# Optimization experiments

Measured on AMD Instinct MI355X. Metric: run time of the kernel, lower is better.

## Reference

```python
import jax, jax.numpy as jnp
import numpy as np

N = 100000   # nodes
E = 800000   # edges (avg degree 8)
IN = 128     # in_dim
H = 128      # hidden_dim
L = 3        # num_layers
EPS = 1e-5   # torch LayerNorm default


def setup_inputs() -> dict:
    key = jax.random.key(0)
    ks = jax.random.split(key, 10)
    s = 0.05
    # DAG edge list: src < dst guarantees acyclicity and node N-1 is a sink.
    rng = np.random.default_rng(0)
    src = rng.integers(0, N - 1, size=E)
    dst = src + 1 + (rng.random(E) * (N - 1 - src)).astype(np.int64)
    return {
        "node_feats": jax.random.normal(ks[0], (N, IN), jnp.float32),
        "src": jnp.asarray(src, jnp.int32),
        "dst": jnp.asarray(dst, jnp.int32),
        "W_in": jax.random.normal(ks[1], (IN, H), jnp.float32) * s,
        "b_in": jnp.zeros((H,), jnp.float32),
        "Ws": jax.random.normal(ks[2], (L, H, H), jnp.float32) * s,
        "bs": jnp.zeros((L, H), jnp.float32),
        "Wn": jax.random.normal(ks[3], (L, H, H), jnp.float32) * s,
        "bn": jnp.zeros((L, H), jnp.float32),
        "Wg": jax.random.normal(ks[4], (L, 2 * H, H), jnp.float32) * s,
        "bg": jnp.zeros((L, H), jnp.float32),
        "gamma": jnp.ones((L, H), jnp.float32),
        "beta": jnp.zeros((L, H), jnp.float32),
        "W_att": jax.random.normal(ks[5], (H, H), jnp.float32) * s,
        "b_att": jnp.zeros((H,), jnp.float32),
        "W_score": jax.random.normal(ks[6], (H, 1), jnp.float32) * s,
        "b_score": jnp.zeros((1,), jnp.float32),
    }


def reference(node_feats, src, dst, W_in, b_in, Ws, bs, Wn, bn, Wg, bg,
              gamma, beta, W_att, b_att, W_score, b_score):
    n = node_feats.shape[0]
    ones_e = jnp.ones(src.shape, node_feats.dtype)
    indeg = jax.ops.segment_sum(ones_e, dst, num_segments=n)          # [N]
    has_pred = (indeg > 0).astype(node_feats.dtype)[:, None]          # [N,1]
    inv_deg = (1.0 / jnp.maximum(indeg, 1.0))[:, None]                # [N,1]
    outdeg = jax.ops.segment_sum(ones_e, src, num_segments=n)
    sink_mask = outdeg == 0                                           # [N]

    h = node_feats @ W_in + b_in                                      # [N,H]
    for i in range(Ws.shape[0]):
        hs = h @ Ws[i] + bs[i]
        # predecessor mean of layer-input h (no within-layer recurrence)
        neigh = jax.ops.segment_sum(h[src], dst, num_segments=n) * inv_deg
        hn = neigh @ Wn[i] + bn[i]
        m = hs + has_pred * hn  # nodes with no preds use m = hs only (bias too)
        gate = jax.nn.sigmoid(jnp.concatenate([h, m], axis=-1) @ Wg[i] + bg[i])
        v = gate * m + (1.0 - gate) * h
        mu = v.mean(-1, keepdims=True)
        var = ((v - mu) ** 2).mean(-1, keepdims=True)
        v = (v - mu) * jax.lax.rsqrt(var + EPS) * gamma[i] + beta[i]
        h = jax.nn.relu(v)

    # attention pooling over sink nodes only
    a = jnp.tanh(h @ W_att + b_att)
    scores = (a @ W_score)[:, 0] + b_score[0]
    scores = jnp.where(sink_mask, scores, -jnp.inf)
    w = jax.nn.softmax(scores, axis=0)  # zero weight on non-sinks
    graph_emb = (w[:, None] * h).sum(0)
    return h, graph_emb
```

## Files before the change

### kernel.cpp

```cpp
#include <hip/hip_runtime.h>
#include <cmath>

typedef unsigned short u16;
typedef unsigned int   u32;
typedef __attribute__((ext_vector_type(8))) short bf16x8;
typedef __attribute__((ext_vector_type(4))) float f32x4;
typedef __attribute__((ext_vector_type(4))) u32   u32x4;

__device__ __forceinline__ float bf2f(u16 u){
    union { u32 i; float f; } x; x.i = ((u32)u) << 16; return x.f;
}
__device__ __forceinline__ u16 f2bf(float f){
    union { float f; u32 i; } x; x.f = f;
    u32 r = x.i + 0x7fffu + ((x.i >> 16) & 1u);
    return (u16)(r >> 16);
}

__device__ __forceinline__ size_t frag_idx(int n, int k){
    int t = n >> 4, sl = n & 15, kk = k >> 5, g16 = (k >> 3) & 3, e = k & 7;
    return ((size_t)(t*4 + kk)*64 + g16*16 + sl)*8 + e;
}


__global__ void k_count(const int* __restrict__ src, const int* __restrict__ dst,
                        int* cnt, int* notsink, int* pos, int E){
    int e = blockIdx.x*256 + threadIdx.x;
    if (e < E){
        pos[e] = atomicAdd(&cnt[dst[e]], 1);
        notsink[src[e]] = 1;
    }
}

__global__ void k_sinklist(const int* __restrict__ notsink, int* sink_list,
                           int* nsink, int N){
    int i = blockIdx.x*256 + threadIdx.x;
    if (i < N && notsink[i] == 0){
        int p = atomicAdd(nsink, 1);
        sink_list[p] = i;
    }
}

__global__ void k_scan1(const int* __restrict__ in, int* blocksum, int N){
    __shared__ int sh[256];
    int tid = threadIdx.x;
    int base = blockIdx.x*1024 + tid*4;
    int s = 0;
    for (int j=0;j<4;j++){ int i = base+j; s += (i < N) ? in[i] : 0; }
    sh[tid] = s; __syncthreads();
    for (int d=128; d>0; d>>=1){ if (tid < d) sh[tid] += sh[tid+d]; __syncthreads(); }
    if (tid == 0) blocksum[blockIdx.x] = sh[0];
}

__global__ void k_scan2(int* blocksum, int nb){
    if (threadIdx.x == 0){
        int run = 0;
        for (int i=0;i<nb;i++){ int v = blocksum[i]; blocksum[i] = run; run += v; }
    }
}

__global__ void k_scan3(const int* __restrict__ in, const int* __restrict__ blockoff,
                        int* out, float* inv_deg, float* haspred, int N){
    __shared__ int sh[256];
    int tid = threadIdx.x;
    int base = blockIdx.x*1024 + tid*4;
    int e[4]; int s = 0;
    for (int j=0;j<4;j++){ int i = base+j; e[j] = (i < N) ? in[i] : 0; s += e[j]; }
    sh[tid] = s; __syncthreads();
    for (int d=1; d<256; d<<=1){
        int t = (tid >= d) ? sh[tid-d] : 0;
        __syncthreads();
        sh[tid] += t;
        __syncthreads();
    }
    int excl = sh[tid] - s + blockoff[blockIdx.x];
    for (int j=0;j<4;j++){
        int i = base+j;
        if (i < N){
            out[i] = excl; excl += e[j];
            inv_deg[i] = 1.0f / (float)(e[j] > 1 ? e[j] : 1);
            haspred[i] = e[j] > 0 ? 1.0f : 0.0f;
        }
    }
}

__global__ void k_place(const int* __restrict__ src, const int* __restrict__ dst,
                        const int* __restrict__ row_ptr, const int* __restrict__ pos,
                        int* csr_src, int E){
    int e = blockIdx.x*256 + threadIdx.x;
    if (e < E)
        csr_src[row_ptr[dst[e]] + pos[e]] = src[e];
}

__global__ void k_wt_plain(const float* __restrict__ W_in, const float* __restrict__ W_att,
                           const float* __restrict__ Ws, const float* __restrict__ Wn,
                           u16* WT_in, u16* WT_att, u16* WB){
    int i = blockIdx.x*256 + threadIdx.x;
    if (i < 32768){
        const float* srcm = (i < 16384) ? W_in : W_att;
        u16* dstm = (i < 16384) ? WT_in : WT_att;
        int w = i & 16383, n = w >> 7, k = w & 127;
        dstm[n*128 + k] = f2bf(srcm[k*128 + n]);
    } else {
        int off = i - 32768;
        int m  = off / 49152;
        int w  = off % 49152;
        int l  = w >> 14, ww = w & 16383;
        int n  = ww >> 7, k = ww & 127;
        const float* srcm = m ? Wn : Ws;
        u16* dstm = WB + ((size_t)l*2 + m)*32768;
        dstm[frag_idx(n, k)] = f2bf(srcm[(size_t)l*16384 + k*128 + n]);
    }
}

__global__ void k_wt_comp(const float* __restrict__ Ws, const float* __restrict__ Wn,
                          const float* __restrict__ Wg,
                          const float* __restrict__ bs, const float* __restrict__ bn,
                          u16* WB, float* vb){
    __shared__ float cols[2][128];
    int l = blockIdx.x / 129;
    int b = blockIdx.x % 129;
    const float* Wgb = Wg + (size_t)l*32768 + 16384;
    int tid = threadIdx.x;
    if (b == 128){
        int n = tid & 127;
        const float* bv = (tid < 128) ? (bs + l*128) : (bn + l*128);
        float acc = 0.f;
        for (int j=0;j<128;j++) acc += bv[j] * Wgb[j*128 + n];
        vb[l*256 + (tid>>7)*128 + n] = acc;
        return;
    }
    int m  = b >> 6;
    int n0 = (b & 63) * 2;
    int nn = tid >> 7, k = tid & 127;
    cols[tid>>7][tid&127] = Wgb[(size_t)(tid&127)*128 + n0 + (tid>>7)];
    __syncthreads();
    const float* A = (m ? Wn : Ws) + (size_t)l*16384;
    float acc = 0.f;
    for (int j=0;j<128;j++) acc += A[k*128 + j] * cols[nn][j];
    int n = n0 + nn;
    if (m == 0) acc += Wg[(size_t)l*32768 + k*128 + n];
    u16* dstm = WB + ((size_t)l*2 + m)*32768;
    dstm[frag_idx(128 + n, k)] = f2bf(acc);
}


__global__ void k_neigh(const u16* __restrict__ h, const int* __restrict__ row_ptr,
                        const int* __restrict__ indeg, const float* __restrict__ inv_deg,
                        const int* __restrict__ csr_src, u16* __restrict__ neigh, int N){
    int wid  = (blockIdx.x*256 + threadIdx.x) >> 6;
    int lane = threadIdx.x & 63;
    int sub = lane >> 4, sl = lane & 15;
    int node = wid*4 + sub;
    bool valid = node < N;
    int deg   = valid ? indeg[node]   : 0;
    int start = valid ? row_ptr[node] : 0;
    float acc[8] = {0.f,0.f,0.f,0.f,0.f,0.f,0.f,0.f};
    for (int e0 = 0; __any(e0 < deg); e0 += 16){
        int idx = 0;
        if (e0 + sl < deg) idx = csr_src[start + e0 + sl];
        int cnt = deg - e0;
        #pragma unroll
        for (int j = 0; j < 16; j++){
            int sidx = __shfl(idx, (sub << 4) | j);
            if (j < cnt){
                bf16x8 v = *(const bf16x8*)(h + (size_t)sidx*128 + sl*8);
                #pragma unroll
                for (int t=0;t<8;t++) acc[t] += bf2f((u16)v[t]);
            }
        }
    }
    if (valid){
        float iv = inv_deg[node];
        u16 o[8];
        #pragma unroll
        for (int t=0;t<8;t++) o[t] = f2bf(acc[t]*iv);
        *(u32x4*)(neigh + (size_t)node*128 + sl*8) = *(const u32x4*)o;
    }
}


__device__ __forceinline__ void stage_A_f32(const float* __restrict__ A, u16 (*lA)[136],
                                            int row0, int n_rows, int tid){
    #pragma unroll
    for (int i=0;i<4;i++){
        int c = i*256 + tid;
        int r = c >> 4, col8 = (c & 15) * 8;
        u16 o[8] = {0,0,0,0,0,0,0,0};
        if (row0 + r < n_rows){
            float4 v0 = *(const float4*)(A + (size_t)(row0 + r)*128 + col8);
            float4 v1 = *(const float4*)(A + (size_t)(row0 + r)*128 + col8 + 4);
            o[0]=f2bf(v0.x); o[1]=f2bf(v0.y); o[2]=f2bf(v0.z); o[3]=f2bf(v0.w);
            o[4]=f2bf(v1.x); o[5]=f2bf(v1.y); o[6]=f2bf(v1.z); o[7]=f2bf(v1.w);
        }
        *(u32x4*)&lA[r][col8] = *(const u32x4*)o;
    }
}

__device__ __forceinline__ void stage_B(const u16* __restrict__ BT, int Ks, int koff0,
                                        u16 (*lB)[136], int tid){
    #pragma unroll
    for (int i=0;i<8;i++){
        int c = i*256 + tid;
        int n = c >> 4, col8 = (c & 15) * 8;
        u32x4 v = *(const u32x4*)(BT + (size_t)n*Ks + koff0 + col8);
        *(u32x4*)&lB[n][col8] = v;
    }
}

__device__ __forceinline__ void mfma_tile(const u16 (*lA)[136], const u16 (*lB)[136],
                                          int wave, int lane, f32x4* acc){
    #pragma unroll
    for (int kk=0;kk<4;kk++){
        int koff = kk*32 + (lane >> 4) * 8;
        bf16x8 a = *(const bf16x8*)&lA[wave*16 + (lane & 15)][koff];
        #pragma unroll
        for (int t=0;t<8;t++){
            bf16x8 b = *(const bf16x8*)&lB[t*16 + (lane & 15)][koff];
            acc[t] = __builtin_amdgcn_mfma_f32_16x16x32_bf16(a, b, acc[t], 0, 0, 0);
        }
    }
}


__global__ __launch_bounds__(256) void k_gemm_in(
    const float* __restrict__ A, const u16* __restrict__ BT,
    const float* __restrict__ bias, u16* __restrict__ C, int n_rows)
{
    __shared__ u16 lA[64][136];
    __shared__ u16 lB[128][136];
    int tid = threadIdx.x, wave = tid >> 6, lane = tid & 63;
    int row0 = blockIdx.x * 64;
    f32x4 acc[8];
    #pragma unroll
    for (int t=0;t<8;t++) acc[t] = (f32x4){0.f,0.f,0.f,0.f};
    stage_A_f32(A, lA, row0, n_rows, tid);
    stage_B(BT, 128, 0, lB, tid);
    __syncthreads();
    mfma_tile(lA, lB, wave, lane, acc);

    int sl = lane & 15;
    int rbase = wave*16 + (lane >> 4)*4;
    float bc[8];
    #pragma unroll
    for (int t=0;t<8;t++) bc[t] = bias[t*16 + sl];
    for (int r=0;r<4;r++){
        int row = row0 + rbase + r;
        if (row >= n_rows) continue;
        #pragma unroll
        for (int t=0;t<8;t++)
            C[(size_t)row*128 + t*16 + sl] = f2bf(acc[t][r] + bc[t]);
    }
}


__global__ __launch_bounds__(256, 3) void k_layer(
    const u16* __restrict__ H, const u16* __restrict__ Ng,
    const u16* __restrict__ WB,
    const float* __restrict__ bs, const float* __restrict__ bn,
    const float* __restrict__ bg,
    const float* __restrict__ vb1, const float* __restrict__ vb2,
    const float* __restrict__ gamma, const float* __restrict__ beta,
    const float* __restrict__ haspred,
    u16* __restrict__ Hb, float* __restrict__ Hf, int n_rows)
{
    __shared__ u16 lH[64][132];
    __shared__ u16 lB[2][8192];
    int tid = threadIdx.x, wave = tid >> 6, lane = tid & 63;
    int sl = lane & 15, g16 = lane >> 4;
    int row0 = blockIdx.x * 64;

    int arow = row0 + wave*16 + sl;
    bool av = arow < n_rows;
    bf16x8 a1[4], a2[4];
    #pragma unroll
    for (int kk=0;kk<4;kk++){
        a1[kk] = (bf16x8){0,0,0,0,0,0,0,0};
        a2[kk] = (bf16x8){0,0,0,0,0,0,0,0};
    }
    if (av){
        #pragma unroll
        for (int kk=0;kk<4;kk++){
            a1[kk] = *(const bf16x8*)(H  + (size_t)arow*128 + kk*32 + g16*8);
            a2[kk] = *(const bf16x8*)(Ng + (size_t)arow*128 + kk*32 + g16*8);
        }
    }

    #pragma unroll
    for (int i=0;i<4;i++){
        int c = i*256 + tid;
        int r = c >> 4, col8 = (c & 15) * 8;
        u32x4 v = {0,0,0,0};
        if (row0 + r < n_rows)
            v = *(const u32x4*)(H + (size_t)(row0 + r)*128 + col8);
        *(u32x4*)&lH[r][col8] = v;
    }

    u32x4 st[4];
    #pragma unroll
    for (int i=0;i<4;i++)
        st[i] = *(const u32x4*)(WB + (size_t)(i*256 + tid)*8);
    #pragma unroll
    for (int i=0;i<4;i++)
        *(u32x4*)&lB[0][(i*256 + tid)*8] = st[i];

    f32x4 acc[16];
    #pragma unroll
    for (int t=0;t<16;t++) acc[t] = (f32x4){0.f,0.f,0.f,0.f};
    __syncthreads();

    #pragma unroll
    for (int s=0;s<8;s++){
        int cur = s & 1;
        if (s < 7){
            const u16* sp = WB + (size_t)(s+1)*8192;
            #pragma unroll
            for (int i=0;i<4;i++)
                st[i] = *(const u32x4*)(sp + (size_t)(i*256 + tid)*8);
        }
        const u16* bp = &lB[cur][lane*8];
        #pragma unroll
        for (int j=0;j<4;j++){
            #pragma unroll
            for (int kk=0;kk<4;kk++){
                bf16x8 b = *(const bf16x8*)(bp + ((j*4 + kk) << 9));
                int ai = (s & 3)*4 + j;
                acc[ai] = __builtin_amdgcn_mfma_f32_16x16x32_bf16(
                    (s >= 4) ? a2[kk] : a1[kk], b, acc[ai], 0, 0, 0);
            }
        }
        if (s < 7){
            #pragma unroll
            for (int i=0;i<4;i++)
                *(u32x4*)&lB[cur ^ 1][(i*256 + tid)*8] = st[i];
        }
        __syncthreads();
    }

    int rbase = wave*16 + g16*4;
    float bM[8], bnl[8], bG[8], vb2l[8], gam[8], bet[8];
    #pragma unroll
    for (int t=0;t<8;t++){
        int c = t*16 + sl;
        bM[t] = bs[c]; bnl[t] = bn[c];
        bG[t] = bg[c] + vb1[c]; vb2l[t] = vb2[c];
        gam[t] = gamma[c]; bet[t] = beta[c];
    }
    for (int r=0;r<4;r++){
        int row = row0 + rbase + r;
        if (row >= n_rows) continue;
        float hp = haspred[row];
        float v[8], s = 0.f;
        #pragma unroll
        for (int t=0;t<8;t++){
            int c = t*16 + sl;
            float m = acc[t][r]   + bM[t] + hp*bnl[t];
            float x = acc[t+8][r] + bG[t] + hp*vb2l[t];
            float gg = 1.f/(1.f + expf(-x));
            float hv = bf2f(lH[rbase + r][c]);
            v[t] = gg*m + (1.f - gg)*hv;
            s += v[t];
        }
        s += __shfl_xor(s,1); s += __shfl_xor(s,2); s += __shfl_xor(s,4); s += __shfl_xor(s,8);
        float mu = s * (1.f/128.f);
        float q = 0.f;
        #pragma unroll
        for (int t=0;t<8;t++){ float d = v[t]-mu; q += d*d; }
        q += __shfl_xor(q,1); q += __shfl_xor(q,2); q += __shfl_xor(q,4); q += __shfl_xor(q,8);
        float rs = rsqrtf(q*(1.f/128.f) + 1e-5f);
        #pragma unroll
        for (int t=0;t<8;t++){
            size_t idx = (size_t)row*128 + t*16 + sl;
            float o = (v[t]-mu)*rs*gam[t] + bet[t];
            o = o > 0.f ? o : 0.f;
            Hb[idx] = f2bf(o);
            if (Hf) Hf[idx] = o;
        }
    }
}


__global__ __launch_bounds__(256) void k_att_sink(
    const u16* __restrict__ H, const u16* __restrict__ BT,
    const float* __restrict__ b_att, const float* __restrict__ Wsc,
    const float* __restrict__ bsc, const int* __restrict__ sink_list,
    const int* __restrict__ nsink, float* __restrict__ scores_sink)
{
    __shared__ u16 lA[64][136];
    __shared__ u16 lB[128][136];
    int ns = *nsink;
    int tid = threadIdx.x, wave = tid >> 6, lane = tid & 63;
    int sl = lane & 15;
    stage_B(BT, 128, 0, lB, tid);
    float bac[8], wc[8];
    #pragma unroll
    for (int t=0;t<8;t++){ bac[t] = b_att[t*16 + sl]; wc[t] = Wsc[t*16 + sl]; }
    float b0 = bsc[0];
    int rbase = wave*16 + (lane >> 4)*4;

    for (int c0 = blockIdx.x*64; c0 < ns; c0 += gridDim.x*64){
        __syncthreads();
        #pragma unroll
        for (int i=0;i<4;i++){
            int c = i*256 + tid;
            int r = c >> 4, col8 = (c & 15) * 8;
            u32x4 v = {0,0,0,0};
            if (c0 + r < ns){
                int row = sink_list[c0 + r];
                v = *(const u32x4*)(H + (size_t)row*128 + col8);
            }
            *(u32x4*)&lA[r][col8] = v;
        }
        __syncthreads();
        f32x4 acc[8];
        #pragma unroll
        for (int t=0;t<8;t++) acc[t] = (f32x4){0.f,0.f,0.f,0.f};
        mfma_tile(lA, lB, wave, lane, acc);

        for (int r=0;r<4;r++){
            int i = c0 + rbase + r;
            if (i >= ns) continue;
            float p = 0.f;
            #pragma unroll
            for (int t=0;t<8;t++) p += tanhf(acc[t][r] + bac[t]) * wc[t];
            p += __shfl_xor(p,1); p += __shfl_xor(p,2); p += __shfl_xor(p,4); p += __shfl_xor(p,8);
            if (sl == 0)
                scores_sink[i] = p + b0;
        }
    }
}


__global__ void k_pool_sink(const u16* __restrict__ h, const int* __restrict__ sink_list,
                            const int* __restrict__ nsink,
                            const float* __restrict__ scores_sink,
                            float* __restrict__ out){
    __shared__ float sh[256];
    __shared__ float swg[2];
    int ns = *nsink;
    int tid = threadIdx.x;
    int col = tid & 127, grp = tid >> 7;
    float acc = 0.f, wsum = 0.f;
    for (int i = grp; i < ns; i += 2){
        float w = expf(scores_sink[i]);
        acc += w * bf2f(h[(size_t)sink_list[i]*128 + col]);
        if (col == 0) wsum += w;
    }
    sh[tid] = acc;
    if (col == 0) swg[grp] = wsum;
    __syncthreads();
    if (tid < 128) out[tid] = (sh[tid] + sh[tid+128]) / (swg[0] + swg[1]);
}


extern "C" void kernel_launch(void* const* d_in, const int* in_sizes, int n_in,
                              void* d_out, int out_size, void* d_ws, size_t ws_size,
                              hipStream_t stream)
{
    const float* node_feats = (const float*)d_in[0];
    const int* src     = (const int*)d_in[1];
    const int* dst     = (const int*)d_in[2];
    const float* W_in    = (const float*)d_in[3];
    const float* b_in    = (const float*)d_in[4];
    const float* Ws      = (const float*)d_in[5];
    const float* bs      = (const float*)d_in[6];
    const float* Wn      = (const float*)d_in[7];
    const float* bn      = (const float*)d_in[8];
    const float* Wg      = (const float*)d_in[9];
    const float* bg      = (const float*)d_in[10];
    const float* gamma   = (const float*)d_in[11];
    const float* beta    = (const float*)d_in[12];
    const float* W_att   = (const float*)d_in[13];
    const float* b_att   = (const float*)d_in[14];
    const float* W_score = (const float*)d_in[15];
    const float* b_score = (const float*)d_in[16];

    const int N = in_sizes[0] / 128;
    const int E = in_sizes[1];

    char* w = (char*)d_ws;
    auto alloc = [&](size_t bytes)->char* {
        char* p = w; w += (bytes + 255) & ~(size_t)255; return p;
    };
    u16* WT_in  = (u16*)alloc(128*128*2);
    u16* WT_att = (u16*)alloc(128*128*2);
    u16* WB     = (u16*)alloc(3*2*256*128*2);
    float* vb   = (float*)alloc(3*256*4);
    int* cnt      = (int*)alloc((size_t)N*4);
    int* notsink  = (int*)alloc((size_t)N*4);
    int* nsink    = (int*)alloc(256);
    size_t zero_bytes = (size_t)((char*)nsink + 256 - (char*)cnt);
    int* pos      = (int*)alloc((size_t)E*4);
    int* row_ptr  = (int*)alloc((size_t)N*4);
    int* blocksum = (int*)alloc(1024*4);
    int* csr_src  = (int*)alloc((size_t)E*4);
    float* inv_deg = (float*)alloc((size_t)N*4);
    float* haspred = (float*)alloc((size_t)N*4);
    int* sink_list = (int*)alloc((size_t)N*4);
    float* scores_sink = (float*)alloc((size_t)N*4);
    u16* buf0 = (u16*)alloc((size_t)N*128*2);
    u16* buf1 = (u16*)alloc((size_t)N*128*2);
    u16* bufn = (u16*)alloc((size_t)N*128*2);

    float* h_out   = (float*)d_out;
    float* emb_out = h_out + (size_t)N*128;

    hipMemsetAsync(cnt, 0, zero_bytes, stream);

    k_wt_plain<<<512, 256, 0, stream>>>(W_in, W_att, Ws, Wn, WT_in, WT_att, WB);
    k_wt_comp<<<3*129, 256, 0, stream>>>(Ws, Wn, Wg, bs, bn, WB, vb);

    k_count<<<(E+255)/256, 256, 0, stream>>>(src, dst, cnt, notsink, pos, E);
    k_sinklist<<<(N+255)/256, 256, 0, stream>>>(notsink, sink_list, nsink, N);

    int nb = (N + 1023) / 1024;
    k_scan1<<<nb, 256, 0, stream>>>(cnt, blocksum, N);
    k_scan2<<<1, 256, 0, stream>>>(blocksum, nb);
    k_scan3<<<nb, 256, 0, stream>>>(cnt, blocksum, row_ptr, inv_deg, haspred, N);
    k_place<<<(E+255)/256, 256, 0, stream>>>(src, dst, row_ptr, pos, csr_src, E);

    int gblk = (N + 63) / 64;
    int nblk = (N + 15) / 16;

    k_gemm_in<<<gblk, 256, 0, stream>>>(node_feats, WT_in, b_in, buf0, N);

    u16* hin = buf0;
    for (int i=0;i<3;i++){
        k_neigh<<<nblk, 256, 0, stream>>>(hin, row_ptr, cnt, inv_deg, csr_src, bufn, N);
        u16* hb  = (hin == buf0) ? buf1 : buf0;
        float* hf = (i == 2) ? h_out : nullptr;
        k_layer<<<gblk, 256, 0, stream>>>(hin, bufn,
                                          WB + (size_t)i*65536,
                                          bs + i*128, bn + i*128, bg + i*128,
                                          vb + i*256, vb + i*256 + 128,
                                          gamma + i*128, beta + i*128, haspred,
                                          hb, hf, N);
        hin = hb;
    }

    k_att_sink<<<8, 256, 0, stream>>>(hin, WT_att, b_att, W_score, b_score,
                                      sink_list, nsink, scores_sink);
    k_pool_sink<<<1, 256, 0, stream>>>(hin, sink_list, nsink, scores_sink, emb_out);

    (void)n_in; (void)out_size; (void)ws_size;
}
```

Before: 531.5 us.

## Fuse neighbor mean aggregation into layer kernel, dropping separate neighbor pass

Removes the standalone neighbor-gather kernel and the intermediate neighbor buffer, computing the predecessor mean inside the layer kernel directly into the MFMA A-fragment registers. Each lane gathers its row's predecessors two edges at a time, loading bf16x8 slices per k-chunk. It also fills the shared H tile from the already-loaded fragments instead of re-reading global memory. This saves a kernel launch and a write plus read of an N x 128 bf16 buffer per layer, but changes gather parallelism (per-row serial loop, divergent degrees within a wave) and adds register pressure under launch bounds of 3 blocks.

```diff
diff --git a/kernel.cpp b/kernel.cpp
--- a/kernel.cpp
+++ b/kernel.cpp
@@ -144,41 +144,6 @@
 }
 
 
-__global__ void k_neigh(const u16* __restrict__ h, const int* __restrict__ row_ptr,
-                        const int* __restrict__ indeg, const float* __restrict__ inv_deg,
-                        const int* __restrict__ csr_src, u16* __restrict__ neigh, int N){
-    int wid  = (blockIdx.x*256 + threadIdx.x) >> 6;
-    int lane = threadIdx.x & 63;
-    int sub = lane >> 4, sl = lane & 15;
-    int node = wid*4 + sub;
-    bool valid = node < N;
-    int deg   = valid ? indeg[node]   : 0;
-    int start = valid ? row_ptr[node] : 0;
-    float acc[8] = {0.f,0.f,0.f,0.f,0.f,0.f,0.f,0.f};
-    for (int e0 = 0; __any(e0 < deg); e0 += 16){
-        int idx = 0;
-        if (e0 + sl < deg) idx = csr_src[start + e0 + sl];
-        int cnt = deg - e0;
-        #pragma unroll
-        for (int j = 0; j < 16; j++){
-            int sidx = __shfl(idx, (sub << 4) | j);
-            if (j < cnt){
-                bf16x8 v = *(const bf16x8*)(h + (size_t)sidx*128 + sl*8);
-                #pragma unroll
-                for (int t=0;t<8;t++) acc[t] += bf2f((u16)v[t]);
-            }
-        }
-    }
-    if (valid){
-        float iv = inv_deg[node];
-        u16 o[8];
-        #pragma unroll
-        for (int t=0;t<8;t++) o[t] = f2bf(acc[t]*iv);
-        *(u32x4*)(neigh + (size_t)node*128 + sl*8) = *(const u32x4*)o;
-    }
-}
-
-
 __device__ __forceinline__ void stage_A_f32(const float* __restrict__ A, u16 (*lA)[136],
                                             int row0, int n_rows, int tid){
     #pragma unroll
@@ -254,8 +219,10 @@
 
 
 __global__ __launch_bounds__(256, 3) void k_layer(
-    const u16* __restrict__ H, const u16* __restrict__ Ng,
+    const u16* __restrict__ H,
     const u16* __restrict__ WB,
+    const int* __restrict__ row_ptr, const int* __restrict__ indeg,
+    const float* __restrict__ inv_deg, const int* __restrict__ csr_src,
     const float* __restrict__ bs, const float* __restrict__ bn,
     const float* __restrict__ bg,
     const float* __restrict__ vb1, const float* __restrict__ vb2,
@@ -271,34 +238,73 @@
 
     int arow = row0 + wave*16 + sl;
     bool av = arow < n_rows;
-    bf16x8 a1[4], a2[4];
-    #pragma unroll
-    for (int kk=0;kk<4;kk++){
-        a1[kk] = (bf16x8){0,0,0,0,0,0,0,0};
-        a2[kk] = (bf16x8){0,0,0,0,0,0,0,0};
-    }
+
+    bf16x8 a1[4];
+    #pragma unroll
+    for (int kk=0;kk<4;kk++) a1[kk] = (bf16x8){0,0,0,0,0,0,0,0};
     if (av){
         #pragma unroll
-        for (int kk=0;kk<4;kk++){
-            a1[kk] = *(const bf16x8*)(H  + (size_t)arow*128 + kk*32 + g16*8);
-            a2[kk] = *(const bf16x8*)(Ng + (size_t)arow*128 + kk*32 + g16*8);
-        }
-    }
-
-    #pragma unroll
-    for (int i=0;i<4;i++){
-        int c = i*256 + tid;
-        int r = c >> 4, col8 = (c & 15) * 8;
-        u32x4 v = {0,0,0,0};
-        if (row0 + r < n_rows)
-            v = *(const u32x4*)(H + (size_t)(row0 + r)*128 + col8);
-        *(u32x4*)&lH[r][col8] = v;
+        for (int kk=0;kk<4;kk++)
+            a1[kk] = *(const bf16x8*)(H + (size_t)arow*128 + kk*32 + g16*8);
     }
 
     u32x4 st[4];
     #pragma unroll
     for (int i=0;i<4;i++)
         st[i] = *(const u32x4*)(WB + (size_t)(i*256 + tid)*8);
+
+    int deg   = av ? indeg[arow]   : 0;
+    int start = av ? row_ptr[arow] : 0;
+    float iv  = av ? inv_deg[arow] : 0.f;
+
+    float ga[4][8];
+    #pragma unroll
+    for (int kk=0;kk<4;kk++)
+        #pragma unroll
+        for (int t=0;t<8;t++) ga[kk][t] = 0.f;
+    for (int e = 0; __any(e < deg); e += 2){
+        bool p0 = e < deg, p1 = e + 1 < deg;
+        int i0 = 0, i1 = 0;
+        if (p0) i0 = csr_src[start + e];
+        if (p1) i1 = csr_src[start + e + 1];
+        bf16x8 v0[4], v1[4];
+        if (p0){
+            #pragma unroll
+            for (int kk=0;kk<4;kk++)
+                v0[kk] = *(const bf16x8*)(H + (size_t)i0*128 + kk*32 + g16*8);
+        }
+        if (p1){
+            #pragma unroll
+            for (int kk=0;kk<4;kk++)
+                v1[kk] = *(const bf16x8*)(H + (size_t)i1*128 + kk*32 + g16*8);
+        }
+        if (p0){
+            #pragma unroll
+            for (int kk=0;kk<4;kk++)
+                #pragma unroll
+                for (int t=0;t<8;t++) ga[kk][t] += bf2f((u16)v0[kk][t]);
+        }
+        if (p1){
+            #pragma unroll
+            for (int kk=0;kk<4;kk++)
+                #pragma unroll
+                for (int t=0;t<8;t++) ga[kk][t] += bf2f((u16)v1[kk][t]);
+        }
+    }
+    bf16x8 a2[4];
+    #pragma unroll
+    for (int kk=0;kk<4;kk++){
+        union { u16 o[8]; bf16x8 v; } cv;
+        #pragma unroll
+        for (int t=0;t<8;t++) cv.o[t] = f2bf(ga[kk][t] * iv);
+        a2[kk] = cv.v;
+    }
+
+    #pragma unroll
+    for (int kk=0;kk<4;kk++){
+        union { bf16x8 v; u32x4 u; } cv; cv.v = a1[kk];
+        *(u32x4*)&lH[wave*16 + sl][kk*32 + g16*8] = cv.u;
+    }
     #pragma unroll
     for (int i=0;i<4;i++)
         *(u32x4*)&lB[0][(i*256 + tid)*8] = st[i];
@@ -499,7 +505,6 @@
     float* scores_sink = (float*)alloc((size_t)N*4);
     u16* buf0 = (u16*)alloc((size_t)N*128*2);
     u16* buf1 = (u16*)alloc((size_t)N*128*2);
-    u16* bufn = (u16*)alloc((size_t)N*128*2);
 
     float* h_out   = (float*)d_out;
     float* emb_out = h_out + (size_t)N*128;
@@ -519,17 +524,16 @@
     k_place<<<(E+255)/256, 256, 0, stream>>>(src, dst, row_ptr, pos, csr_src, E);
 
     int gblk = (N + 63) / 64;
-    int nblk = (N + 15) / 16;
 
     k_gemm_in<<<gblk, 256, 0, stream>>>(node_feats, WT_in, b_in, buf0, N);
 
     u16* hin = buf0;
     for (int i=0;i<3;i++){
-        k_neigh<<<nblk, 256, 0, stream>>>(hin, row_ptr, cnt, inv_deg, csr_src, bufn, N);
         u16* hb  = (hin == buf0) ? buf1 : buf0;
         float* hf = (i == 2) ? h_out : nullptr;
-        k_layer<<<gblk, 256, 0, stream>>>(hin, bufn,
+        k_layer<<<gblk, 256, 0, stream>>>(hin,
                                           WB + (size_t)i*65536,
+                                          row_ptr, cnt, inv_deg, csr_src,
                                           bs + i*128, bn + i*128, bg + i*128,
                                           vb + i*256, vb + i*256 + 128,
                                           gamma + i*128, beta + i*128, haspred,
```

Result: slower. 566.8 us (+6.6%).

## Re-tile layer GEMM so each wave owns column slices and reads weights from global

Applied to the files above, without the earlier changes.

The fused layer kernel changes from a row-per-wave split with double-buffered LDS weight staging to one where each wave owns 32 output columns across all 64 rows. Both H and the neighbor tile are staged in LDS as A operands, and weight fragments are loaded directly from global/L2 without LDS staging or per-stage barriers. LayerNorm statistics now need a cross-wave reduction through shared memory and use a one-pass sum/sum-of-squares variance, which is slightly less numerically robust. The aim is to cut the eight barrier-synchronised staging steps and LDS weight traffic, in exchange for more global weight reads per block and an extra barrier.

```diff
diff --git a/kernel.cpp b/kernel.cpp
--- a/kernel.cpp
+++ b/kernel.cpp
@@ -90,6 +90,7 @@
     if (e < E)
         csr_src[row_ptr[dst[e]] + pos[e]] = src[e];
 }
+
 
 __global__ void k_wt_plain(const float* __restrict__ W_in, const float* __restrict__ W_att,
                            const float* __restrict__ Ws, const float* __restrict__ Wn,
@@ -179,6 +180,19 @@
 }
 
 
+__device__ __forceinline__ void stage_A_bf16(const u16* __restrict__ A, u16 (*lA)[136],
+                                             int row0, int n_rows, int tid){
+    #pragma unroll
+    for (int i=0;i<4;i++){
+        int c = i*256 + tid;
+        int r = c >> 4, col8 = (c & 15) * 8;
+        u32x4 v = {0,0,0,0};
+        if (row0 + r < n_rows)
+            v = *(const u32x4*)(A + (size_t)(row0 + r)*128 + col8);
+        *(u32x4*)&lA[r][col8] = v;
+    }
+}
+
 __device__ __forceinline__ void stage_A_f32(const float* __restrict__ A, u16 (*lA)[136],
                                             int row0, int n_rows, int tid){
     #pragma unroll
@@ -255,7 +269,7 @@
 
 __global__ __launch_bounds__(256, 3) void k_layer(
     const u16* __restrict__ H, const u16* __restrict__ Ng,
-    const u16* __restrict__ WB,
+    const u16* __restrict__ WB1, const u16* __restrict__ WB2,
     const float* __restrict__ bs, const float* __restrict__ bn,
     const float* __restrict__ bg,
     const float* __restrict__ vb1, const float* __restrict__ vb2,
@@ -263,117 +277,119 @@
     const float* __restrict__ haspred,
     u16* __restrict__ Hb, float* __restrict__ Hf, int n_rows)
 {
-    __shared__ u16 lH[64][132];
-    __shared__ u16 lB[2][8192];
+    __shared__ u16 lA[64][132];
+    __shared__ u16 lN[64][132];
+    __shared__ float redS[64][4];
+    __shared__ float redQ[64][4];
     int tid = threadIdx.x, wave = tid >> 6, lane = tid & 63;
     int sl = lane & 15, g16 = lane >> 4;
     int row0 = blockIdx.x * 64;
 
-    int arow = row0 + wave*16 + sl;
-    bool av = arow < n_rows;
-    bf16x8 a1[4], a2[4];
-    #pragma unroll
-    for (int kk=0;kk<4;kk++){
-        a1[kk] = (bf16x8){0,0,0,0,0,0,0,0};
-        a2[kk] = (bf16x8){0,0,0,0,0,0,0,0};
-    }
-    if (av){
-        #pragma unroll
-        for (int kk=0;kk<4;kk++){
-            a1[kk] = *(const bf16x8*)(H  + (size_t)arow*128 + kk*32 + g16*8);
-            a2[kk] = *(const bf16x8*)(Ng + (size_t)arow*128 + kk*32 + g16*8);
-        }
-    }
-
     #pragma unroll
     for (int i=0;i<4;i++){
         int c = i*256 + tid;
         int r = c >> 4, col8 = (c & 15) * 8;
-        u32x4 v = {0,0,0,0};
-        if (row0 + r < n_rows)
-            v = *(const u32x4*)(H + (size_t)(row0 + r)*128 + col8);
-        *(u32x4*)&lH[r][col8] = v;
-    }
-
-    u32x4 st[4];
-    #pragma unroll
-    for (int i=0;i<4;i++)
-        st[i] = *(const u32x4*)(WB + (size_t)(i*256 + tid)*8);
-    #pragma unroll
-    for (int i=0;i<4;i++)
-        *(u32x4*)&lB[0][(i*256 + tid)*8] = st[i];
-
-    f32x4 acc[16];
-    #pragma unroll
-    for (int t=0;t<16;t++) acc[t] = (f32x4){0.f,0.f,0.f,0.f};
+        u32x4 va = {0,0,0,0}, vn = {0,0,0,0};
+        if (row0 + r < n_rows){
+            va = *(const u32x4*)(H  + (size_t)(row0 + r)*128 + col8);
+            vn = *(const u32x4*)(Ng + (size_t)(row0 + r)*128 + col8);
+        }
+        *(u32x4*)&lA[r][col8] = va;
+        *(u32x4*)&lN[r][col8] = vn;
+    }
     __syncthreads();
 
-    #pragma unroll
-    for (int s=0;s<8;s++){
-        int cur = s & 1;
-        if (s < 7){
-            const u16* sp = WB + (size_t)(s+1)*8192;
+    f32x4 accM[2][4], accG[2][4];
+    #pragma unroll
+    for (int ct=0;ct<2;ct++)
+        #pragma unroll
+        for (int rt=0;rt<4;rt++){
+            accM[ct][rt] = (f32x4){0.f,0.f,0.f,0.f};
+            accG[ct][rt] = (f32x4){0.f,0.f,0.f,0.f};
+        }
+
+    #pragma unroll
+    for (int m=0;m<2;m++){
+        const u16* Wm = m ? WB2 : WB1;
+        const u16 (*lX)[132] = m ? lN : lA;
+        #pragma unroll
+        for (int kk=0;kk<4;kk++){
+            bf16x8 a[4];
             #pragma unroll
-            for (int i=0;i<4;i++)
-                st[i] = *(const u32x4*)(sp + (size_t)(i*256 + tid)*8);
-        }
-        const u16* bp = &lB[cur][lane*8];
-        #pragma unroll
-        for (int j=0;j<4;j++){
+            for (int rt=0;rt<4;rt++)
+                a[rt] = *(const bf16x8*)&lX[rt*16 + sl][kk*32 + g16*8];
             #pragma unroll
-            for (int kk=0;kk<4;kk++){
-                bf16x8 b = *(const bf16x8*)(bp + ((j*4 + kk) << 9));
-                int ai = (s & 3)*4 + j;
-                acc[ai] = __builtin_amdgcn_mfma_f32_16x16x32_bf16(
-                    (s >= 4) ? a2[kk] : a1[kk], b, acc[ai], 0, 0, 0);
+            for (int ct=0;ct<2;ct++){
+                int tM = 2*wave + ct, tG = 8 + 2*wave + ct;
+                bf16x8 bM = *(const bf16x8*)(Wm + ((size_t)(tM*4 + kk)*64 + lane)*8);
+                bf16x8 bG = *(const bf16x8*)(Wm + ((size_t)(tG*4 + kk)*64 + lane)*8);
+                #pragma unroll
+                for (int rt=0;rt<4;rt++){
+                    accM[ct][rt] = __builtin_amdgcn_mfma_f32_16x16x32_bf16(a[rt], bM, accM[ct][rt], 0, 0, 0);
+                    accG[ct][rt] = __builtin_amdgcn_mfma_f32_16x16x32_bf16(a[rt], bG, accG[ct][rt], 0, 0, 0);
+                }
             }
         }
-        if (s < 7){
+    }
+
+    int c0 = 32*wave + sl;
+    float bM_[2], bnl[2], bG_[2], vb2_[2], gam[2], bet[2];
+    #pragma unroll
+    for (int ct=0;ct<2;ct++){
+        int c = c0 + ct*16;
+        bM_[ct] = bs[c]; bnl[ct] = bn[c];
+        bG_[ct] = bg[c] + vb1[c]; vb2_[ct] = vb2[c];
+        gam[ct] = gamma[c]; bet[ct] = beta[c];
+    }
+
+    float v[2][4][4];
+    #pragma unroll
+    for (int rt=0;rt<4;rt++){
+        #pragma unroll
+        for (int r=0;r<4;r++){
+            int row = rt*16 + g16*4 + r;
+            float hp = (row0 + row < n_rows) ? haspred[row0 + row] : 0.f;
+            float s = 0.f, q = 0.f;
             #pragma unroll
-            for (int i=0;i<4;i++)
-                *(u32x4*)&lB[cur ^ 1][(i*256 + tid)*8] = st[i];
-        }
-        __syncthreads();
-    }
-
-    int rbase = wave*16 + g16*4;
-    float bM[8], bnl[8], bG[8], vb2l[8], gam[8], bet[8];
-    #pragma unroll
-    for (int t=0;t<8;t++){
-        int c = t*16 + sl;
-        bM[t] = bs[c]; bnl[t] = bn[c];
-        bG[t] = bg[c] + vb1[c]; vb2l[t] = vb2[c];
-        gam[t] = gamma[c]; bet[t] = beta[c];
-    }
-    for (int r=0;r<4;r++){
-        int row = row0 + rbase + r;
-        if (row >= n_rows) continue;
-        float hp = haspred[row];
-        float v[8], s = 0.f;
-        #pragma unroll
-        for (int t=0;t<8;t++){
-            int c = t*16 + sl;
-            float m = acc[t][r]   + bM[t] + hp*bnl[t];
-            float x = acc[t+8][r] + bG[t] + hp*vb2l[t];
-            float gg = 1.f/(1.f + expf(-x));
-            float hv = bf2f(lH[rbase + r][c]);
-            v[t] = gg*m + (1.f - gg)*hv;
-            s += v[t];
-        }
-        s += __shfl_xor(s,1); s += __shfl_xor(s,2); s += __shfl_xor(s,4); s += __shfl_xor(s,8);
-        float mu = s * (1.f/128.f);
-        float q = 0.f;
-        #pragma unroll
-        for (int t=0;t<8;t++){ float d = v[t]-mu; q += d*d; }
-        q += __shfl_xor(q,1); q += __shfl_xor(q,2); q += __shfl_xor(q,4); q += __shfl_xor(q,8);
-        float rs = rsqrtf(q*(1.f/128.f) + 1e-5f);
-        #pragma unroll
-        for (int t=0;t<8;t++){
-            size_t idx = (size_t)row*128 + t*16 + sl;
-            float o = (v[t]-mu)*rs*gam[t] + bet[t];
-            o = o > 0.f ? o : 0.f;
-            Hb[idx] = f2bf(o);
-            if (Hf) Hf[idx] = o;
+            for (int ct=0;ct<2;ct++){
+                float mval = accM[ct][rt][r] + bM_[ct] + hp*bnl[ct];
+                float x    = accG[ct][rt][r] + bG_[ct] + hp*vb2_[ct];
+                float gg = 1.f/(1.f + expf(-x));
+                float hv = bf2f(lA[row][c0 + ct*16]);
+                float vv = gg*mval + (1.f - gg)*hv;
+                v[ct][rt][r] = vv;
+                s += vv; q += vv*vv;
+            }
+            s += __shfl_xor(s,1); s += __shfl_xor(s,2); s += __shfl_xor(s,4); s += __shfl_xor(s,8);
+            q += __shfl_xor(q,1); q += __shfl_xor(q,2); q += __shfl_xor(q,4); q += __shfl_xor(q,8);
+            if (sl == rt){
+                redS[row][wave] = s;
+                redQ[row][wave] = q;
+            }
+        }
+    }
+    __syncthreads();
+
+    #pragma unroll
+    for (int rt=0;rt<4;rt++){
+        #pragma unroll
+        for (int r=0;r<4;r++){
+            int row = rt*16 + g16*4 + r;
+            if (row0 + row >= n_rows) continue;
+            float4 ss = *(const float4*)redS[row];
+            float4 qq = *(const float4*)redQ[row];
+            float mu  = (ss.x + ss.y + ss.z + ss.w) * (1.f/128.f);
+            float var = (qq.x + qq.y + qq.z + qq.w) * (1.f/128.f) - mu*mu;
+            float rs = rsqrtf(var + 1e-5f);
+            #pragma unroll
+            for (int ct=0;ct<2;ct++){
+                int col = c0 + ct*16;
+                float o = (v[ct][rt][r] - mu)*rs*gam[ct] + bet[ct];
+                o = o > 0.f ? o : 0.f;
+                size_t idx = (size_t)(row0 + row)*128 + col;
+                Hb[idx] = f2bf(o);
+                if (Hf) Hf[idx] = o;
+            }
         }
     }
 }
@@ -529,7 +545,7 @@
         u16* hb  = (hin == buf0) ? buf1 : buf0;
         float* hf = (i == 2) ? h_out : nullptr;
         k_layer<<<gblk, 256, 0, stream>>>(hin, bufn,
-                                          WB + (size_t)i*65536,
+                                          WB + (size_t)i*65536, WB + (size_t)i*65536 + 32768,
                                           bs + i*128, bn + i*128, bg + i*128,
                                           vb + i*256, vb + i*256 + 128,
                                           gamma + i*128, beta + i*128, haspred,
```

Result: slower. 587.8 us (+10.6%).

## Process 128 rows per k_layer block to reuse staged weight tiles

Applied to the files above, without the earlier changes.

Each k_layer block now handles 128 rows instead of 64: every wave holds two 16-row A fragment groups and issues two MFMAs per B fragment read from LDS. This halves the number of times the 64K-element weight block is streamed from global memory into LDS across the grid, and the H tile in LDS is now filled from the A-fragment registers instead of a separate global load. The cost is doubled accumulator registers (occupancy hint lowered from 3 to 2 blocks per CU), a larger LDS footprint, and about half as many blocks.

```diff
diff --git a/kernel.cpp b/kernel.cpp
--- a/kernel.cpp
+++ b/kernel.cpp
@@ -90,6 +90,7 @@
     if (e < E)
         csr_src[row_ptr[dst[e]] + pos[e]] = src[e];
 }
+
 
 __global__ void k_wt_plain(const float* __restrict__ W_in, const float* __restrict__ W_att,
                            const float* __restrict__ Ws, const float* __restrict__ Wn,
@@ -253,7 +254,7 @@
 }
 
 
-__global__ __launch_bounds__(256, 3) void k_layer(
+__global__ __launch_bounds__(256, 2) void k_layer(
     const u16* __restrict__ H, const u16* __restrict__ Ng,
     const u16* __restrict__ WB,
     const float* __restrict__ bs, const float* __restrict__ bn,
@@ -263,49 +264,52 @@
     const float* __restrict__ haspred,
     u16* __restrict__ Hb, float* __restrict__ Hf, int n_rows)
 {
-    __shared__ u16 lH[64][132];
+    __shared__ u16 lH[128][132];
     __shared__ u16 lB[2][8192];
     int tid = threadIdx.x, wave = tid >> 6, lane = tid & 63;
     int sl = lane & 15, g16 = lane >> 4;
-    int row0 = blockIdx.x * 64;
-
-    int arow = row0 + wave*16 + sl;
-    bool av = arow < n_rows;
-    bf16x8 a1[4], a2[4];
-    #pragma unroll
-    for (int kk=0;kk<4;kk++){
-        a1[kk] = (bf16x8){0,0,0,0,0,0,0,0};
-        a2[kk] = (bf16x8){0,0,0,0,0,0,0,0};
-    }
-    if (av){
+    int row0 = blockIdx.x * 128;
+
+    bf16x8 a1[2][4], a2[2][4];
+    #pragma unroll
+    for (int rg=0;rg<2;rg++){
+        int arow = row0 + wave*32 + rg*16 + sl;
+        bool av = arow < n_rows;
         #pragma unroll
         for (int kk=0;kk<4;kk++){
-            a1[kk] = *(const bf16x8*)(H  + (size_t)arow*128 + kk*32 + g16*8);
-            a2[kk] = *(const bf16x8*)(Ng + (size_t)arow*128 + kk*32 + g16*8);
-        }
-    }
-
-    #pragma unroll
-    for (int i=0;i<4;i++){
-        int c = i*256 + tid;
-        int r = c >> 4, col8 = (c & 15) * 8;
-        u32x4 v = {0,0,0,0};
-        if (row0 + r < n_rows)
-            v = *(const u32x4*)(H + (size_t)(row0 + r)*128 + col8);
-        *(u32x4*)&lH[r][col8] = v;
+            a1[rg][kk] = (bf16x8){0,0,0,0,0,0,0,0};
+            a2[rg][kk] = (bf16x8){0,0,0,0,0,0,0,0};
+        }
+        if (av){
+            #pragma unroll
+            for (int kk=0;kk<4;kk++){
+                a1[rg][kk] = *(const bf16x8*)(H  + (size_t)arow*128 + kk*32 + g16*8);
+                a2[rg][kk] = *(const bf16x8*)(Ng + (size_t)arow*128 + kk*32 + g16*8);
+            }
+        }
     }
 
     u32x4 st[4];
     #pragma unroll
     for (int i=0;i<4;i++)
         st[i] = *(const u32x4*)(WB + (size_t)(i*256 + tid)*8);
+
+    #pragma unroll
+    for (int rg=0;rg<2;rg++)
+        #pragma unroll
+        for (int kk=0;kk<4;kk++){
+            union { bf16x8 v; u32x4 u; } cv; cv.v = a1[rg][kk];
+            *(u32x4*)&lH[wave*32 + rg*16 + sl][kk*32 + g16*8] = cv.u;
+        }
     #pragma unroll
     for (int i=0;i<4;i++)
         *(u32x4*)&lB[0][(i*256 + tid)*8] = st[i];
 
-    f32x4 acc[16];
-    #pragma unroll
-    for (int t=0;t<16;t++) acc[t] = (f32x4){0.f,0.f,0.f,0.f};
+    f32x4 acc[2][16];
+    #pragma unroll
+    for (int rg=0;rg<2;rg++)
+        #pragma unroll
+        for (int t=0;t<16;t++) acc[rg][t] = (f32x4){0.f,0.f,0.f,0.f};
     __syncthreads();
 
     #pragma unroll
@@ -324,8 +328,13 @@
             for (int kk=0;kk<4;kk++){
                 bf16x8 b = *(const bf16x8*)(bp + ((j*4 + kk) << 9));
                 int ai = (s & 3)*4 + j;
-                acc[ai] = __builtin_amdgcn_mfma_f32_16x16x32_bf16(
-                    (s >= 4) ? a2[kk] : a1[kk], b, acc[ai], 0, 0, 0);
+                if (s < 4){
+                    acc[0][ai] = __builtin_amdgcn_mfma_f32_16x16x32_bf16(a1[0][kk], b, acc[0][ai], 0, 0, 0);
+                    acc[1][ai] = __builtin_amdgcn_mfma_f32_16x16x32_bf16(a1[1][kk], b, acc[1][ai], 0, 0, 0);
+                } else {
+                    acc[0][ai] = __builtin_amdgcn_mfma_f32_16x16x32_bf16(a2[0][kk], b, acc[0][ai], 0, 0, 0);
+                    acc[1][ai] = __builtin_amdgcn_mfma_f32_16x16x32_bf16(a2[1][kk], b, acc[1][ai], 0, 0, 0);
+                }
             }
         }
         if (s < 7){
@@ -336,7 +345,6 @@
         __syncthreads();
     }
 
-    int rbase = wave*16 + g16*4;
     float bM[8], bnl[8], bG[8], vb2l[8], gam[8], bet[8];
     #pragma unroll
     for (int t=0;t<8;t++){
@@ -345,35 +353,39 @@
         bG[t] = bg[c] + vb1[c]; vb2l[t] = vb2[c];
         gam[t] = gamma[c]; bet[t] = beta[c];
     }
-    for (int r=0;r<4;r++){
-        int row = row0 + rbase + r;
-        if (row >= n_rows) continue;
-        float hp = haspred[row];
-        float v[8], s = 0.f;
-        #pragma unroll
-        for (int t=0;t<8;t++){
-            int c = t*16 + sl;
-            float m = acc[t][r]   + bM[t] + hp*bnl[t];
-            float x = acc[t+8][r] + bG[t] + hp*vb2l[t];
-            float gg = 1.f/(1.f + expf(-x));
-            float hv = bf2f(lH[rbase + r][c]);
-            v[t] = gg*m + (1.f - gg)*hv;
-            s += v[t];
-        }
-        s += __shfl_xor(s,1); s += __shfl_xor(s,2); s += __shfl_xor(s,4); s += __shfl_xor(s,8);
-        float mu = s * (1.f/128.f);
-        float q = 0.f;
-        #pragma unroll
-        for (int t=0;t<8;t++){ float d = v[t]-mu; q += d*d; }
-        q += __shfl_xor(q,1); q += __shfl_xor(q,2); q += __shfl_xor(q,4); q += __shfl_xor(q,8);
-        float rs = rsqrtf(q*(1.f/128.f) + 1e-5f);
-        #pragma unroll
-        for (int t=0;t<8;t++){
-            size_t idx = (size_t)row*128 + t*16 + sl;
-            float o = (v[t]-mu)*rs*gam[t] + bet[t];
-            o = o > 0.f ? o : 0.f;
-            Hb[idx] = f2bf(o);
-            if (Hf) Hf[idx] = o;
+    #pragma unroll
+    for (int rg=0;rg<2;rg++){
+        int rbase = wave*32 + rg*16 + g16*4;
+        for (int r=0;r<4;r++){
+            int row = row0 + rbase + r;
+            if (row >= n_rows) continue;
+            float hp = haspred[row];
+            float v[8], s = 0.f;
+            #pragma unroll
+            for (int t=0;t<8;t++){
+                int c = t*16 + sl;
+                float m = acc[rg][t][r]   + bM[t] + hp*bnl[t];
+                float x = acc[rg][t+8][r] + bG[t] + hp*vb2l[t];
+                float gg = 1.f/(1.f + expf(-x));
+                float hv = bf2f(lH[rbase + r][c]);
+                v[t] = gg*m + (1.f - gg)*hv;
+                s += v[t];
+            }
+            s += __shfl_xor(s,1); s += __shfl_xor(s,2); s += __shfl_xor(s,4); s += __shfl_xor(s,8);
+            float mu = s * (1.f/128.f);
+            float q = 0.f;
+            #pragma unroll
+            for (int t=0;t<8;t++){ float d = v[t]-mu; q += d*d; }
+            q += __shfl_xor(q,1); q += __shfl_xor(q,2); q += __shfl_xor(q,4); q += __shfl_xor(q,8);
+            float rs = rsqrtf(q*(1.f/128.f) + 1e-5f);
+            #pragma unroll
+            for (int t=0;t<8;t++){
+                size_t idx = (size_t)row*128 + t*16 + sl;
+                float o = (v[t]-mu)*rs*gam[t] + bet[t];
+                o = o > 0.f ? o : 0.f;
+                Hb[idx] = f2bf(o);
+                if (Hf) Hf[idx] = o;
+            }
         }
     }
 }
@@ -518,8 +530,9 @@
     k_scan3<<<nb, 256, 0, stream>>>(cnt, blocksum, row_ptr, inv_deg, haspred, N);
     k_place<<<(E+255)/256, 256, 0, stream>>>(src, dst, row_ptr, pos, csr_src, E);
 
-    int gblk = (N + 63) / 64;
-    int nblk = (N + 15) / 16;
+    int gblk  = (N + 63) / 64;
+    int lblk  = (N + 127) / 128;
+    int nblk  = (N + 15) / 16;
 
     k_gemm_in<<<gblk, 256, 0, stream>>>(node_feats, WT_in, b_in, buf0, N);
 
@@ -528,7 +541,7 @@
         k_neigh<<<nblk, 256, 0, stream>>>(hin, row_ptr, cnt, inv_deg, csr_src, bufn, N);
         u16* hb  = (hin == buf0) ? buf1 : buf0;
         float* hf = (i == 2) ? h_out : nullptr;
-        k_layer<<<gblk, 256, 0, stream>>>(hin, bufn,
+        k_layer<<<lblk, 256, 0, stream>>>(hin, bufn,
                                           WB + (size_t)i*65536,
                                           bs + i*128, bn + i*128, bg + i*128,
                                           vb + i*256, vb + i*256 + 128,
```

Result: slower. 543.9 us (+2.3%).
